# Performance work log

Hardware: AMD Instinct MI355X
Metric: run time of the kernel (lower is better)

## Reference

```python
import jax, jax.numpy as jnp
import numpy as np

N = 100000
E = 1600000
IN = 256
H = 4
D = 32           # n_hidden per head
C = 47           # n_classes per head in last layer
NEG_SLOPE = 0.2


def setup_inputs() -> dict:
    key = jax.random.key(0)
    ks = jax.random.split(key, 20)
    x = jax.random.normal(ks[0], (N, IN), dtype=jnp.float32)
    src = jax.random.randint(ks[1], (E,), 0, N, dtype=jnp.int32)
    dst = jax.random.randint(ks[2], (E,), 0, N, dtype=jnp.int32)
    s = 0.05
    inp = {"x": x, "src": src, "dst": dst}
    # layer 0: in 256 -> (H=4, D=32)
    inp["W0s"] = jax.random.normal(ks[3], (IN, H * D), dtype=jnp.float32) * s
    inp["W0d"] = jax.random.normal(ks[4], (IN, H * D), dtype=jnp.float32) * s
    inp["a0l"] = jax.random.normal(ks[5], (H, D), dtype=jnp.float32) * s
    inp["a0r"] = jax.random.normal(ks[6], (H, D), dtype=jnp.float32) * s
    inp["b0"] = jnp.zeros((H, D), dtype=jnp.float32)
    # layer 1: in 128 -> (4, 32)
    inp["W1s"] = jax.random.normal(ks[7], (H * D, H * D), dtype=jnp.float32) * s
    inp["W1d"] = jax.random.normal(ks[8], (H * D, H * D), dtype=jnp.float32) * s
    inp["a1l"] = jax.random.normal(ks[9], (H, D), dtype=jnp.float32) * s
    inp["a1r"] = jax.random.normal(ks[10], (H, D), dtype=jnp.float32) * s
    inp["b1"] = jnp.zeros((H, D), dtype=jnp.float32)
    # layer 2: in 128 -> (4, 47), no activation
    inp["W2s"] = jax.random.normal(ks[11], (H * D, H * C), dtype=jnp.float32) * s
    inp["W2d"] = jax.random.normal(ks[12], (H * D, H * C), dtype=jnp.float32) * s
    inp["a2l"] = jax.random.normal(ks[13], (H, C), dtype=jnp.float32) * s
    inp["a2r"] = jax.random.normal(ks[14], (H, C), dtype=jnp.float32) * s
    inp["b2"] = jnp.zeros((H, C), dtype=jnp.float32)
    return inp


def _gat_layer(h, src, dst, Ws, Wd, al, ar, b):
    # h: [N, F_in]; full-graph block so h_dst == h
    n = h.shape[0]
    heads, dout = al.shape
    fs = (h @ Ws).reshape(n, heads, dout)   # [N, H, D]
    fd = (h @ Wd).reshape(n, heads, dout)
    el = jnp.sum(fs * al, axis=-1)          # [N, H]
    er = jnp.sum(fd * ar, axis=-1)
    e = el[src] + er[dst]                   # [E, H]
    e = jnp.where(e > 0, e, NEG_SLOPE * e)  # leaky_relu
    # segment softmax over incoming edges of each dst node
    m = jax.lax.stop_gradient(jax.ops.segment_max(e, dst, num_segments=n))
    ez = jnp.exp(e - m[dst])
    denom = jax.ops.segment_sum(ez, dst, num_segments=n)
    alpha = ez / denom[dst]                 # [E, H]
    msg = fs[src] * alpha[:, :, None]       # [E, H, D]
    rst = jax.ops.segment_sum(msg, dst, num_segments=n)  # [N, H, D]
    return rst + b


def reference(x, src, dst,
              W0s, W0d, a0l, a0r, b0,
              W1s, W1d, a1l, a1r, b1,
              W2s, W2d, a2l, a2r, b2):
    h = _gat_layer(x, src, dst, W0s, W0d, a0l, a0r, b0)
    h = jax.nn.relu(h).reshape(h.shape[0], -1)           # flatten(1)
    h = _gat_layer(h, src, dst, W1s, W1d, a1l, a1r, b1)
    h = jax.nn.relu(h).reshape(h.shape[0], -1)
    h = _gat_layer(h, src, dst, W2s, W2d, a2l, a2r, b2)  # [N, H, C]
    h = h.mean(axis=1)                                   # mean over heads
    return jax.nn.log_softmax(h, axis=-1)
```

## Files before the change

### kernel.cpp

```cpp
#include <hip/hip_runtime.h>
#include <math.h>

#define NEG_SLOPE 0.2f

typedef _Float16 half2v __attribute__((ext_vector_type(2)));
typedef _Float16 half8 __attribute__((ext_vector_type(8)));
typedef float float4v __attribute__((ext_vector_type(4)));
typedef float float2v __attribute__((ext_vector_type(2)));

__device__ __forceinline__ float lrelu(float x) { return x > 0.f ? x : NEG_SLOPE * x; }

__device__ __forceinline__ float sel4(const float4 v, int h) {
  float r = v.x;
  r = (h == 1) ? v.y : r;
  r = (h == 2) ? v.z : r;
  r = (h == 3) ? v.w : r;
  return r;
}

__device__ __forceinline__ unsigned char f32_to_fp8(float a) {
  int v = __builtin_amdgcn_cvt_pk_fp8_f32(a, 0.f, 0, false);
  return (unsigned char)(v & 0xff);
}


__global__ void k_hist(const int* __restrict__ dst, int* __restrict__ cnt, int E) {
  int i = blockIdx.x * blockDim.x + threadIdx.x;
  if (i < E) atomicAdd(&cnt[dst[i]], 1);
}

__global__ __launch_bounds__(256) void k_offsets(const int* __restrict__ cnt,
                                                 int* __restrict__ row_start,
                                                 int* __restrict__ gcount, int N) {
  __shared__ int s[256];
  __shared__ int base;
  int tid = threadIdx.x;
  int i = blockIdx.x * 256 + tid;
  int c = (i < N) ? cnt[i] : 0;
  s[tid] = c;
  __syncthreads();
  for (int off = 1; off < 256; off <<= 1) {
    int v = 0;
    if (tid >= off) v = s[tid - off];
    __syncthreads();
    if (tid >= off) s[tid] += v;
    __syncthreads();
  }
  if (tid == 255) base = atomicAdd(gcount, s[255]);
  __syncthreads();
  if (i < N) row_start[i] = base + s[tid] - c;
}

__global__ void k_scatter(const int* __restrict__ src, const int* __restrict__ dst,
                          const int* __restrict__ row_start, int* __restrict__ fill,
                          int* __restrict__ srcs, int E) {
  int i = blockIdx.x * blockDim.x + threadIdx.x;
  if (i < E) {
    int d = dst[i];
    int p = row_start[d] + atomicAdd(&fill[d], 1);
    srcs[p] = src[i];
  }
}

__device__ __forceinline__ void wlr_one(const float* Ws, const float* Wd,
                                        const float* al, const float* ar,
                                        float* wlr, int K, int Dh, int i) {
  int M = 4 * Dh;
  int k = i >> 2, h = i & 3;
  float sl = 0.f, sr = 0.f;
  for (int d = 0; d < Dh; d++) {
    sl += Ws[(size_t)k * M + h * Dh + d] * al[h * Dh + d];
    sr += Wd[(size_t)k * M + h * Dh + d] * ar[h * Dh + d];
  }
  wlr[k * 8 + h] = sl;
  wlr[k * 8 + 4 + h] = sr;
}

__global__ __launch_bounds__(256) void k_prep(
    const float* __restrict__ W0s, const float* __restrict__ W0d,
    const float* __restrict__ a0l, const float* __restrict__ a0r,
    const float* __restrict__ W1s, const float* __restrict__ W1d,
    const float* __restrict__ a1l, const float* __restrict__ a1r,
    const float* __restrict__ W2s, const float* __restrict__ W2d,
    const float* __restrict__ a2l, const float* __restrict__ a2r,
    float* __restrict__ wlr0, float* __restrict__ wlr1, float* __restrict__ wlr2,
    _Float16* __restrict__ Wt0, _Float16* __restrict__ Wt1, _Float16* __restrict__ Wt2) {
  int i = blockIdx.x * 256 + threadIdx.x;
  if (i < 1024) {
    wlr_one(W0s, W0d, a0l, a0r, wlr0, 256, 32, i);
  } else if (i < 1536) {
    wlr_one(W1s, W1d, a1l, a1r, wlr1, 128, 32, i - 1024);
  } else if (i < 2048) {
    wlr_one(W2s, W2d, a2l, a2r, wlr2, 128, 47, i - 1536);
  } else if (i < 2048 + 32768) {
    int j = i - 2048;
    int m = j >> 8, k = j & 255;
    Wt0[j] = (_Float16)W0s[(size_t)k * 128 + m];
  } else if (i < 2048 + 32768 + 16384) {
    int j = i - (2048 + 32768);
    int m = j >> 7, k = j & 127;
    Wt1[j] = (_Float16)W1s[(size_t)k * 128 + m];
  } else if (i < 2048 + 32768 + 16384 + 24576) {
    int j = i - (2048 + 32768 + 16384);
    int r = j >> 7, k = j & 127;
    int h = r / 48, c = r % 48;
    float v = (c < 47) ? W2s[(size_t)k * 188 + 47 * h + c] : 0.f;
    Wt2[j] = (_Float16)v;
  }
}

template <int BN, typename AT>
__global__ __launch_bounds__(256) void k_gemm_mfma(const AT* __restrict__ A,
                                                   const _Float16* __restrict__ Bt,
                                                   const float* __restrict__ wlr,
                                                   unsigned char* __restrict__ C,
                                                   float* __restrict__ el,
                                                   float* __restrict__ er, int N, int K) {
  constexpr int NT = BN / 64;
  constexpr int ASZ = 4 * 64 * 8;
  constexpr int BSZ = (BN / 16) * 64 * 8;
  constexpr int SSZ = ASZ + BSZ;
  __shared__ __align__(16) _Float16 smem[SSZ];
  __shared__ float swlr[2048];
  _Float16* As = smem;
  _Float16* Bs = smem + ASZ;

  const int tid = threadIdx.x;
  const int lane = tid & 63;
  const int w = tid >> 6;
  const int row0 = blockIdx.x * 64;

  for (int i = tid; i < K * 8; i += 256) swlr[i] = wlr[i];
  __syncthreads();

  float4v acc[4][NT];
#pragma unroll
  for (int i = 0; i < 4; i++)
#pragma unroll
    for (int j = 0; j < NT; j++) acc[i][j] = (float4v){0.f, 0.f, 0.f, 0.f};
  float p[8] = {0, 0, 0, 0, 0, 0, 0, 0};

  const int ar_ = tid >> 2, aq = tid & 3;
  for (int k0 = 0; k0 < K; k0 += 32) {
    {
      int gr = row0 + ar_;
      float a8[8];
      if (gr < N) {
        if constexpr (sizeof(AT) == 4) {
          const float4* pp = (const float4*)&A[(size_t)gr * K + k0 + aq * 8];
          float4 u0 = pp[0], u1 = pp[1];
          a8[0] = u0.x; a8[1] = u0.y; a8[2] = u0.z; a8[3] = u0.w;
          a8[4] = u1.x; a8[5] = u1.y; a8[6] = u1.z; a8[7] = u1.w;
        } else {
          half8 hv = *(const half8*)&A[(size_t)gr * K + k0 + aq * 8];
#pragma unroll
          for (int j = 0; j < 8; j++) a8[j] = (float)hv[j];
        }
      } else {
#pragma unroll
        for (int j = 0; j < 8; j++) a8[j] = 0.f;
      }
      half8 v;
#pragma unroll
      for (int j = 0; j < 8; j++) v[j] = (_Float16)a8[j];
      *(half8*)&As[(size_t)(((ar_ >> 4) * 64) + (ar_ & 15) + 16 * aq) * 8] = v;
#pragma unroll
      for (int j = 0; j < 8; j++) {
        const float av = a8[j];
        const float* wp = &swlr[(k0 + aq * 8 + j) * 8];
        float4 w0 = *(const float4*)wp;
        float4 w1 = *(const float4*)(wp + 4);
        p[0] += av * w0.x; p[1] += av * w0.y; p[2] += av * w0.z; p[3] += av * w0.w;
        p[4] += av * w1.x; p[5] += av * w1.y; p[6] += av * w1.z; p[7] += av * w1.w;
      }
    }
#pragma unroll
    for (int i = 0; i < NT; i++) {
      int idx = tid + i * 256;
      int n = idx >> 2, q = idx & 3;
      half8 v = *(const half8*)&Bt[(size_t)n * K + k0 + q * 8];
      *(half8*)&Bs[(size_t)((n >> 4) * 64 + (n & 15) + 16 * q) * 8] = v;
    }
    __syncthreads();
    half8 af[4];
#pragma unroll
    for (int mt = 0; mt < 4; mt++) af[mt] = *(half8*)&As[(size_t)(mt * 64 + lane) * 8];
#pragma unroll
    for (int nt = 0; nt < NT; nt++) {
      half8 bf = *(half8*)&Bs[(size_t)((w * NT + nt) * 64 + lane) * 8];
#pragma unroll
      for (int mt = 0; mt < 4; mt++)
        acc[mt][nt] = __builtin_amdgcn_mfma_f32_16x16x32_f16(af[mt], bf, acc[mt][nt], 0, 0, 0);
    }
    __syncthreads();
  }

#pragma unroll
  for (int j = 0; j < 8; j++) swlr[(ar_ * 4 + aq) * 8 + j] = p[j];

  unsigned char* cs = (unsigned char*)smem;
  const int quad = lane >> 4;
#pragma unroll
  for (int mt = 0; mt < 4; mt++)
#pragma unroll
    for (int nt = 0; nt < NT; nt++)
#pragma unroll
      for (int reg = 0; reg < 4; reg++) {
        int r = mt * 16 + quad * 4 + reg;
        int cc = (w * NT + nt) * 16 + (lane & 15);
        cs[r * BN + cc] = f32_to_fp8(acc[mt][nt][reg]);
      }
  __syncthreads();
  if (tid < 64) {
    int gr = row0 + tid;
    if (gr < N) {
      float e[8];
#pragma unroll
      for (int j = 0; j < 8; j++)
        e[j] = swlr[(tid * 4 + 0) * 8 + j] + swlr[(tid * 4 + 1) * 8 + j] +
               swlr[(tid * 4 + 2) * 8 + j] + swlr[(tid * 4 + 3) * 8 + j];
      *(float4*)&el[(size_t)gr * 4] = make_float4(e[0], e[1], e[2], e[3]);
      *(float4*)&er[(size_t)gr * 4] = make_float4(e[4], e[5], e[6], e[7]);
    }
  }
  constexpr int PER = (64 * BN) / (256 * 16);
  const uint4* s4 = (const uint4*)cs;
#pragma unroll
  for (int i = 0; i < PER; i++) {
    int idx = tid + i * 256;
    int r = idx / (BN / 16), c16 = idx % (BN / 16);
    int gr = row0 + r;
    if (gr < N) *(uint4*)&C[(size_t)gr * BN + c16 * 16] = s4[idx];
  }
}

__global__ __launch_bounds__(256) void k_edge_mid(
    const unsigned char* __restrict__ F, const float* __restrict__ el,
    const float* __restrict__ er, const int* __restrict__ row_start,
    const int* __restrict__ cnt, const int* __restrict__ srcs,
    const float* __restrict__ bias, _Float16* __restrict__ hout, int N) {
  __shared__ float sEz[4][64][4];
  __shared__ int sU[4][64];
  int lane = threadIdx.x & 63;
  int w = threadIdx.x >> 6;
  int v = blockIdx.x * 4 + w;
  if (v >= N) return;
  int start = row_start[v], deg = cnt[v];
  float4 erv = *(const float4*)&er[(size_t)v * 4];
  const int g = lane >> 4;
  const int fl = lane & 15;
  const int h = fl >> 2;
  float acc[8] = {0, 0, 0, 0, 0, 0, 0, 0};
  float4 lsum = make_float4(0.f, 0.f, 0.f, 0.f);

  for (int c = 0; c < deg; c += 64) {
    int take = min(64, deg - c);
    if (lane < take) {
      int u = srcs[start + c + lane];
      float4 e = *(const float4*)&el[(size_t)u * 4];
      float4 ez;
      ez.x = __expf(lrelu(e.x + erv.x));
      ez.y = __expf(lrelu(e.y + erv.y));
      ez.z = __expf(lrelu(e.z + erv.z));
      ez.w = __expf(lrelu(e.w + erv.w));
      lsum.x += ez.x; lsum.y += ez.y; lsum.z += ez.z; lsum.w += ez.w;
      sU[w][lane] = u;
      *(float4*)&sEz[w][lane][0] = ez;
    }
    for (int kk = g; kk < take; kk += 4) {
      int u = sU[w][kk];
      float ezh = sEz[w][kk][h];
      uint2 d = *(const uint2*)&F[(size_t)u * 128 + 8 * fl];
      float2v c0 = __builtin_amdgcn_cvt_pk_f32_fp8((int)d.x, false);
      float2v c1 = __builtin_amdgcn_cvt_pk_f32_fp8((int)d.x, true);
      float2v c2 = __builtin_amdgcn_cvt_pk_f32_fp8((int)d.y, false);
      float2v c3 = __builtin_amdgcn_cvt_pk_f32_fp8((int)d.y, true);
      acc[0] += ezh * c0.x; acc[1] += ezh * c0.y;
      acc[2] += ezh * c1.x; acc[3] += ezh * c1.y;
      acc[4] += ezh * c2.x; acc[5] += ezh * c2.y;
      acc[6] += ezh * c3.x; acc[7] += ezh * c3.y;
    }
  }
#pragma unroll
  for (int j = 0; j < 8; j++) {
    acc[j] += __shfl_xor(acc[j], 16);
    acc[j] += __shfl_xor(acc[j], 32);
  }
#pragma unroll
  for (int msk = 1; msk < 64; msk <<= 1) {
    lsum.x += __shfl_xor(lsum.x, msk);
    lsum.y += __shfl_xor(lsum.y, msk);
    lsum.z += __shfl_xor(lsum.z, msk);
    lsum.w += __shfl_xor(lsum.w, msk);
  }
  if (g == 0) {
    float inv = (deg > 0) ? 1.f / sel4(lsum, h) : 0.f;
    const float4* bp = (const float4*)&bias[8 * fl];
    float4 b0v = bp[0], b1v = bp[1];
    float bb[8] = {b0v.x, b0v.y, b0v.z, b0v.w, b1v.x, b1v.y, b1v.z, b1v.w};
    half8 o;
#pragma unroll
    for (int j = 0; j < 8; j++) o[j] = (_Float16)fmaxf(fmaf(acc[j], inv, bb[j]), 0.f);
    *(half8*)&hout[(size_t)v * 128 + 8 * fl] = o;
  }
}

__global__ __launch_bounds__(256) void k_edge_final(
    const unsigned char* __restrict__ F, const float* __restrict__ el,
    const float* __restrict__ er, const int* __restrict__ row_start,
    const int* __restrict__ cnt, const int* __restrict__ srcs,
    const float* __restrict__ b2, float* __restrict__ out, int N) {
  __shared__ float sEz[4][64][4];
  __shared__ int sU[4][64];
  __shared__ float red[4][192];
  int lane = threadIdx.x & 63;
  int w = threadIdx.x >> 6;
  int v = blockIdx.x * 4 + w;
  if (v >= N) return;
  int start = row_start[v], deg = cnt[v];
  float4 erv = *(const float4*)&er[(size_t)v * 4];
  const int sub = lane >> 5;
  const int l24 = lane & 31;
  const bool act = l24 < 24;
  const int h = l24 / 6;
  const int j6 = l24 % 6;
  const int foff = 48 * h + 8 * j6;
  float acc[8] = {0, 0, 0, 0, 0, 0, 0, 0};
  float4 lsum = make_float4(0.f, 0.f, 0.f, 0.f);

  for (int c = 0; c < deg; c += 64) {
    int take = min(64, deg - c);
    if (lane < take) {
      int u = srcs[start + c + lane];
      float4 e = *(const float4*)&el[(size_t)u * 4];
      float4 ez;
      ez.x = __expf(lrelu(e.x + erv.x));
      ez.y = __expf(lrelu(e.y + erv.y));
      ez.z = __expf(lrelu(e.z + erv.z));
      ez.w = __expf(lrelu(e.w + erv.w));
      lsum.x += ez.x; lsum.y += ez.y; lsum.z += ez.z; lsum.w += ez.w;
      sU[w][lane] = u;
      *(float4*)&sEz[w][lane][0] = ez;
    }
    if (act) {
      for (int kk = sub; kk < take; kk += 2) {
        int u = sU[w][kk];
        float ezh = sEz[w][kk][h];
        uint2 d = *(const uint2*)&F[(size_t)u * 192 + foff];
        float2v c0 = __builtin_amdgcn_cvt_pk_f32_fp8((int)d.x, false);
        float2v c1 = __builtin_amdgcn_cvt_pk_f32_fp8((int)d.x, true);
        float2v c2 = __builtin_amdgcn_cvt_pk_f32_fp8((int)d.y, false);
        float2v c3 = __builtin_amdgcn_cvt_pk_f32_fp8((int)d.y, true);
        acc[0] += ezh * c0.x; acc[1] += ezh * c0.y;
        acc[2] += ezh * c1.x; acc[3] += ezh * c1.y;
        acc[4] += ezh * c2.x; acc[5] += ezh * c2.y;
        acc[6] += ezh * c3.x; acc[7] += ezh * c3.y;
      }
    }
  }
#pragma unroll
  for (int j = 0; j < 8; j++) acc[j] += __shfl_xor(acc[j], 32);
#pragma unroll
  for (int msk = 1; msk < 64; msk <<= 1) {
    lsum.x += __shfl_xor(lsum.x, msk);
    lsum.y += __shfl_xor(lsum.y, msk);
    lsum.z += __shfl_xor(lsum.z, msk);
    lsum.w += __shfl_xor(lsum.w, msk);
  }
  if (act && sub == 0) {
    float inv = (deg > 0) ? 1.f / sel4(lsum, h) : 0.f;
#pragma unroll
    for (int j = 0; j < 8; j++) {
      int cc = 8 * j6 + j;
      float bv = (cc < 47) ? b2[47 * h + cc] : 0.f;
      red[w][foff + j] = fmaf(acc[j], inv, bv);
    }
  }
  __syncthreads();
  float g = -INFINITY;
  if (lane < 47)
    g = 0.25f * (red[w][lane] + red[w][lane + 48] + red[w][lane + 96] + red[w][lane + 144]);
  float gm = g;
#pragma unroll
  for (int msk = 1; msk < 64; msk <<= 1) gm = fmaxf(gm, __shfl_xor(gm, msk));
  float ex = (lane < 47) ? __expf(g - gm) : 0.f;
  float s = ex;
#pragma unroll
  for (int msk = 1; msk < 64; msk <<= 1) s += __shfl_xor(s, msk);
  if (lane < 47) out[(size_t)v * 47 + lane] = g - gm - __logf(s);
}

extern "C" void kernel_launch(void* const* d_in, const int* in_sizes, int n_in,
                              void* d_out, int out_size, void* d_ws, size_t ws_size,
                              hipStream_t stream) {
  const float* x = (const float*)d_in[0];
  const int* src = (const int*)d_in[1];
  const int* dst = (const int*)d_in[2];
  const float* W0s = (const float*)d_in[3];
  const float* W0d = (const float*)d_in[4];
  const float* a0l = (const float*)d_in[5];
  const float* a0r = (const float*)d_in[6];
  const float* b0 = (const float*)d_in[7];
  const float* W1s = (const float*)d_in[8];
  const float* W1d = (const float*)d_in[9];
  const float* a1l = (const float*)d_in[10];
  const float* a1r = (const float*)d_in[11];
  const float* b1 = (const float*)d_in[12];
  const float* W2s = (const float*)d_in[13];
  const float* W2d = (const float*)d_in[14];
  const float* a2l = (const float*)d_in[15];
  const float* a2r = (const float*)d_in[16];
  const float* b2 = (const float*)d_in[17];
  float* out = (float*)d_out;

  const int N = in_sizes[0] / 256;
  const int E = in_sizes[1];

  char* w = (char*)d_ws;
  size_t off = 0;
  auto alloc = [&](size_t bytes) -> void* {
    void* p = w + off;
    off += (bytes + 255) & ~(size_t)255;
    return p;
  };
  int* gcount = (int*)alloc(4);
  int* cnt = (int*)alloc((size_t)N * 4);
  int* fill = (int*)alloc((size_t)N * 4);
  size_t zbytes = off;
  int* row_start = (int*)alloc((size_t)N * 4);
  int* srcs = (int*)alloc((size_t)E * 4);
  float* wlr0 = (float*)alloc(256 * 8 * 4);
  float* wlr1 = (float*)alloc(128 * 8 * 4);
  float* wlr2 = (float*)alloc(128 * 8 * 4);
  _Float16* Wt0 = (_Float16*)alloc(128 * 256 * 2);
  _Float16* Wt1 = (_Float16*)alloc(128 * 128 * 2);
  _Float16* Wt2 = (_Float16*)alloc(192 * 128 * 2);
  float* el = (float*)alloc((size_t)N * 4 * 4);
  float* er = (float*)alloc((size_t)N * 4 * 4);
  unsigned char* F = (unsigned char*)alloc((size_t)N * 192);
  _Float16* Ha = (_Float16*)alloc((size_t)N * 128 * 2);
  _Float16* Hc = (_Float16*)alloc((size_t)N * 128 * 2);
  (void)ws_size;

  hipMemsetAsync(d_ws, 0, zbytes, stream);
  k_hist<<<(E + 255) / 256, 256, 0, stream>>>(dst, cnt, E);
  k_offsets<<<(N + 255) / 256, 256, 0, stream>>>(cnt, row_start, gcount, N);
  k_scatter<<<(E + 255) / 256, 256, 0, stream>>>(src, dst, row_start, fill, srcs, E);
  k_prep<<<(75776 + 255) / 256, 256, 0, stream>>>(W0s, W0d, a0l, a0r, W1s, W1d, a1l, a1r,
                                                  W2s, W2d, a2l, a2r, wlr0, wlr1, wlr2,
                                                  Wt0, Wt1, Wt2);

  int gemm_grid = (N + 63) / 64;
  int node_grid = (N + 3) / 4;

  k_gemm_mfma<128, float><<<gemm_grid, 256, 0, stream>>>(x, Wt0, wlr0, F, el, er, N, 256);
  k_edge_mid<<<node_grid, 256, 0, stream>>>(F, el, er, row_start, cnt, srcs, b0, Ha, N);

  k_gemm_mfma<128, _Float16><<<gemm_grid, 256, 0, stream>>>(Ha, Wt1, wlr1, F, el, er, N, 128);
  k_edge_mid<<<node_grid, 256, 0, stream>>>(F, el, er, row_start, cnt, srcs, b1, Hc, N);

  k_gemm_mfma<192, _Float16><<<gemm_grid, 256, 0, stream>>>(Hc, Wt2, wlr2, F, el, er, N, 128);
  k_edge_final<<<node_grid, 256, 0, stream>>>(F, el, er, row_start, cnt, srcs, b2, out, N);
}
```

Before: 683.0 us.

## Widen edge gathers to 16-byte loads with software prefetch and packed FMA

The mid and final edge-aggregation kernels now gather 16 fp8 features per lane with uint4 loads instead of 8 with uint2. More edges are handled in parallel per wavefront (8 in the mid kernel, 5 in the final one), and the next edge's row is loaded before the current one is accumulated, using float2 packed multiply-adds. The cross-lane reductions are rebuilt for the new lane mapping, the bias is folded in after the head mean, and the block-wide __syncthreads is dropped. This trades more shuffle reduction steps and idle lanes in the final kernel for fewer, wider memory transactions and more loads in flight. Dropping the barrier across a wave's shared-memory writes and reads relies on wavefront-level ordering.

```diff
diff --git a/kernel.cpp b/kernel.cpp
--- a/kernel.cpp
+++ b/kernel.cpp
@@ -21,6 +21,19 @@
 __device__ __forceinline__ unsigned char f32_to_fp8(float a) {
   int v = __builtin_amdgcn_cvt_pk_fp8_f32(a, 0.f, 0, false);
   return (unsigned char)(v & 0xff);
+}
+
+__device__ __forceinline__ void acc16(float2v acc[8], uint4 d, float ez) {
+  float2v ez2 = {ez, ez};
+  float2v c;
+  c = __builtin_amdgcn_cvt_pk_f32_fp8((int)d.x, false); acc[0] += ez2 * c;
+  c = __builtin_amdgcn_cvt_pk_f32_fp8((int)d.x, true);  acc[1] += ez2 * c;
+  c = __builtin_amdgcn_cvt_pk_f32_fp8((int)d.y, false); acc[2] += ez2 * c;
+  c = __builtin_amdgcn_cvt_pk_f32_fp8((int)d.y, true);  acc[3] += ez2 * c;
+  c = __builtin_amdgcn_cvt_pk_f32_fp8((int)d.z, false); acc[4] += ez2 * c;
+  c = __builtin_amdgcn_cvt_pk_f32_fp8((int)d.z, true);  acc[5] += ez2 * c;
+  c = __builtin_amdgcn_cvt_pk_f32_fp8((int)d.w, false); acc[6] += ez2 * c;
+  c = __builtin_amdgcn_cvt_pk_f32_fp8((int)d.w, true);  acc[7] += ez2 * c;
 }
 
 
@@ -247,10 +260,12 @@
   if (v >= N) return;
   int start = row_start[v], deg = cnt[v];
   float4 erv = *(const float4*)&er[(size_t)v * 4];
-  const int g = lane >> 4;
-  const int fl = lane & 15;
-  const int h = fl >> 2;
-  float acc[8] = {0, 0, 0, 0, 0, 0, 0, 0};
+  const int g8 = lane >> 3;
+  const int sl = lane & 7;
+  const int h = sl >> 1;
+  float2v acc2[8];
+#pragma unroll
+  for (int i = 0; i < 8; i++) acc2[i] = (float2v){0.f, 0.f};
   float4 lsum = make_float4(0.f, 0.f, 0.f, 0.f);
 
   for (int c = 0; c < deg; c += 64) {
@@ -267,25 +282,28 @@
       sU[w][lane] = u;
       *(float4*)&sEz[w][lane][0] = ez;
     }
-    for (int kk = g; kk < take; kk += 4) {
-      int u = sU[w][kk];
-      float ezh = sEz[w][kk][h];
-      uint2 d = *(const uint2*)&F[(size_t)u * 128 + 8 * fl];
-      float2v c0 = __builtin_amdgcn_cvt_pk_f32_fp8((int)d.x, false);
-      float2v c1 = __builtin_amdgcn_cvt_pk_f32_fp8((int)d.x, true);
-      float2v c2 = __builtin_amdgcn_cvt_pk_f32_fp8((int)d.y, false);
-      float2v c3 = __builtin_amdgcn_cvt_pk_f32_fp8((int)d.y, true);
-      acc[0] += ezh * c0.x; acc[1] += ezh * c0.y;
-      acc[2] += ezh * c1.x; acc[3] += ezh * c1.y;
-      acc[4] += ezh * c2.x; acc[5] += ezh * c2.y;
-      acc[6] += ezh * c3.x; acc[7] += ezh * c3.y;
-    }
-  }
-#pragma unroll
-  for (int j = 0; j < 8; j++) {
-    acc[j] += __shfl_xor(acc[j], 16);
-    acc[j] += __shfl_xor(acc[j], 32);
-  }
+    int kk = g8;
+    if (kk < take) {
+      int u0 = sU[w][kk];
+      float ez0 = sEz[w][kk][h];
+      uint4 d0 = *(const uint4*)&F[((unsigned)u0 << 7) + 16u * (unsigned)sl];
+      for (kk += 8; kk < take; kk += 8) {
+        int u1 = sU[w][kk];
+        float ez1 = sEz[w][kk][h];
+        uint4 d1 = *(const uint4*)&F[((unsigned)u1 << 7) + 16u * (unsigned)sl];
+        acc16(acc2, d0, ez0);
+        d0 = d1; ez0 = ez1;
+      }
+      acc16(acc2, d0, ez0);
+    }
+  }
+#pragma unroll
+  for (int m = 8; m < 64; m <<= 1)
+#pragma unroll
+    for (int i = 0; i < 8; i++) {
+      acc2[i].x += __shfl_xor(acc2[i].x, m);
+      acc2[i].y += __shfl_xor(acc2[i].y, m);
+    }
 #pragma unroll
   for (int msk = 1; msk < 64; msk <<= 1) {
     lsum.x += __shfl_xor(lsum.x, msk);
@@ -293,15 +311,25 @@
     lsum.z += __shfl_xor(lsum.z, msk);
     lsum.w += __shfl_xor(lsum.w, msk);
   }
-  if (g == 0) {
+  if (g8 == 0) {
     float inv = (deg > 0) ? 1.f / sel4(lsum, h) : 0.f;
-    const float4* bp = (const float4*)&bias[8 * fl];
-    float4 b0v = bp[0], b1v = bp[1];
-    float bb[8] = {b0v.x, b0v.y, b0v.z, b0v.w, b1v.x, b1v.y, b1v.z, b1v.w};
-    half8 o;
-#pragma unroll
-    for (int j = 0; j < 8; j++) o[j] = (_Float16)fmaxf(fmaf(acc[j], inv, bb[j]), 0.f);
-    *(half8*)&hout[(size_t)v * 128 + 8 * fl] = o;
+    const float4* bp = (const float4*)&bias[16 * sl];
+    float4 b0v = bp[0], b1v = bp[1], b2v = bp[2], b3v = bp[3];
+    float bb[16] = {b0v.x, b0v.y, b0v.z, b0v.w, b1v.x, b1v.y, b1v.z, b1v.w,
+                    b2v.x, b2v.y, b2v.z, b2v.w, b3v.x, b3v.y, b3v.z, b3v.w};
+    half8 o0, o1;
+#pragma unroll
+    for (int j = 0; j < 8; j++) {
+      float a = acc2[j >> 1][j & 1];
+      o0[j] = (_Float16)fmaxf(fmaf(a, inv, bb[j]), 0.f);
+    }
+#pragma unroll
+    for (int j = 0; j < 8; j++) {
+      float a = acc2[(j + 8) >> 1][j & 1];
+      o1[j] = (_Float16)fmaxf(fmaf(a, inv, bb[j + 8]), 0.f);
+    }
+    *(half8*)&hout[(size_t)v * 128 + 16 * sl] = o0;
+    *(half8*)&hout[(size_t)v * 128 + 16 * sl + 8] = o1;
   }
 }
 
@@ -319,13 +347,13 @@
   if (v >= N) return;
   int start = row_start[v], deg = cnt[v];
   float4 erv = *(const float4*)&er[(size_t)v * 4];
-  const int sub = lane >> 5;
-  const int l24 = lane & 31;
-  const bool act = l24 < 24;
-  const int h = l24 / 6;
-  const int j6 = l24 % 6;
-  const int foff = 48 * h + 8 * j6;
-  float acc[8] = {0, 0, 0, 0, 0, 0, 0, 0};
+  const int e0 = lane / 12;
+  const int sl = lane - e0 * 12;
+  const bool act = e0 < 5;
+  const int h = sl / 3;
+  float2v acc2[8];
+#pragma unroll
+  for (int i = 0; i < 8; i++) acc2[i] = (float2v){0.f, 0.f};
   float4 lsum = make_float4(0.f, 0.f, 0.f, 0.f);
 
   for (int c = 0; c < deg; c += 64) {
@@ -343,23 +371,32 @@
       *(float4*)&sEz[w][lane][0] = ez;
     }
     if (act) {
-      for (int kk = sub; kk < take; kk += 2) {
-        int u = sU[w][kk];
-        float ezh = sEz[w][kk][h];
-        uint2 d = *(const uint2*)&F[(size_t)u * 192 + foff];
-        float2v c0 = __builtin_amdgcn_cvt_pk_f32_fp8((int)d.x, false);
-        float2v c1 = __builtin_amdgcn_cvt_pk_f32_fp8((int)d.x, true);
-        float2v c2 = __builtin_amdgcn_cvt_pk_f32_fp8((int)d.y, false);
-        float2v c3 = __builtin_amdgcn_cvt_pk_f32_fp8((int)d.y, true);
-        acc[0] += ezh * c0.x; acc[1] += ezh * c0.y;
-        acc[2] += ezh * c1.x; acc[3] += ezh * c1.y;
-        acc[4] += ezh * c2.x; acc[5] += ezh * c2.y;
-        acc[6] += ezh * c3.x; acc[7] += ezh * c3.y;
+      int kk = e0;
+      if (kk < take) {
+        int u0 = sU[w][kk];
+        float ez0 = sEz[w][kk][h];
+        uint4 d0 = *(const uint4*)&F[(unsigned)u0 * 192u + 16u * (unsigned)sl];
+        for (kk += 5; kk < take; kk += 5) {
+          int u1 = sU[w][kk];
+          float ez1 = sEz[w][kk][h];
+          uint4 d1 = *(const uint4*)&F[(unsigned)u1 * 192u + 16u * (unsigned)sl];
+          acc16(acc2, d0, ez0);
+          d0 = d1; ez0 = ez1;
+        }
+        acc16(acc2, d0, ez0);
       }
     }
   }
 #pragma unroll
-  for (int j = 0; j < 8; j++) acc[j] += __shfl_xor(acc[j], 32);
+  for (int i = 0; i < 8; i++) {
+    float ax = acc2[i].x, ay = acc2[i].y;
+    float t1x = ax + __shfl(ax, lane + 12);
+    float t1y = ay + __shfl(ay, lane + 12);
+    float t2x = t1x + __shfl(t1x, lane + 24);
+    float t2y = t1y + __shfl(t1y, lane + 24);
+    acc2[i].x = t2x + __shfl(ax, lane + 48);
+    acc2[i].y = t2y + __shfl(ay, lane + 48);
+  }
 #pragma unroll
   for (int msk = 1; msk < 64; msk <<= 1) {
     lsum.x += __shfl_xor(lsum.x, msk);
@@ -367,19 +404,20 @@
     lsum.z += __shfl_xor(lsum.z, msk);
     lsum.w += __shfl_xor(lsum.w, msk);
   }
-  if (act && sub == 0) {
+  if (lane < 12) {
     float inv = (deg > 0) ? 1.f / sel4(lsum, h) : 0.f;
 #pragma unroll
     for (int j = 0; j < 8; j++) {
-      int cc = 8 * j6 + j;
-      float bv = (cc < 47) ? b2[47 * h + cc] : 0.f;
-      red[w][foff + j] = fmaf(acc[j], inv, bv);
-    }
-  }
-  __syncthreads();
+      red[w][sl * 16 + 2 * j] = acc2[j].x * inv;
+      red[w][sl * 16 + 2 * j + 1] = acc2[j].y * inv;
+    }
+  }
   float g = -INFINITY;
-  if (lane < 47)
-    g = 0.25f * (red[w][lane] + red[w][lane + 48] + red[w][lane + 96] + red[w][lane + 144]);
+  if (lane < 47) {
+    float s4 = red[w][lane] + red[w][lane + 48] + red[w][lane + 96] + red[w][lane + 144];
+    float bsum = b2[lane] + b2[47 + lane] + b2[94 + lane] + b2[141 + lane];
+    g = 0.25f * (s4 + bsum);
+  }
   float gm = g;
 #pragma unroll
   for (int msk = 1; msk < 64; msk <<= 1) gm = fmaxf(gm, __shfl_xor(gm, msk));
```

Result: slower. 712.8 us (+4.4%).

## Split layer-0 edge aggregation into two head-half passes with cached edge scores

Applied to the files above, without the earlier changes.

Layer 0's edge kernel is split into two passes. Each pass gathers only half of every source node's FP8 feature row (64 of 128 bytes), so the gathered working set per pass is smaller and more likely to stay in cache. The first pass computes the exp scores and stores them with the source index in a packed per-edge buffer that reuses the Hc scratch space, and it writes per-node inverse denominators. The second pass reads the packed buffer for the other two heads instead of recomputing. The cost is an extra launch and extra per-edge writes and reads of the 16-byte packed records.

```diff
diff --git a/kernel.cpp b/kernel.cpp
--- a/kernel.cpp
+++ b/kernel.cpp
@@ -305,6 +305,155 @@
   }
 }
 
+__global__ __launch_bounds__(256) void k_edge_midA(
+    const unsigned char* __restrict__ F, const float* __restrict__ el,
+    const float* __restrict__ er, const int* __restrict__ row_start,
+    const int* __restrict__ cnt, const int* __restrict__ srcs,
+    const float* __restrict__ bias, _Float16* __restrict__ hout,
+    uint4* __restrict__ ezPk, float* __restrict__ invd, int N) {
+  __shared__ float sEz[4][64][2];
+  __shared__ int sU[4][64];
+  int lane = threadIdx.x & 63;
+  int w = threadIdx.x >> 6;
+  int v = blockIdx.x * 4 + w;
+  if (v >= N) return;
+  int start = row_start[v], deg = cnt[v];
+  float4 erv = *(const float4*)&er[(size_t)v * 4];
+  const int g = lane >> 3;
+  const int fl = lane & 7;
+  const int h = fl >> 2;
+  float acc[8] = {0, 0, 0, 0, 0, 0, 0, 0};
+  float4 lsum = make_float4(0.f, 0.f, 0.f, 0.f);
+
+  for (int c = 0; c < deg; c += 64) {
+    int take = min(64, deg - c);
+    if (lane < take) {
+      int u = srcs[start + c + lane];
+      float4 e = *(const float4*)&el[(size_t)u * 4];
+      float4 ez;
+      ez.x = __expf(lrelu(e.x + erv.x));
+      ez.y = __expf(lrelu(e.y + erv.y));
+      ez.z = __expf(lrelu(e.z + erv.z));
+      ez.w = __expf(lrelu(e.w + erv.w));
+      lsum.x += ez.x; lsum.y += ez.y; lsum.z += ez.z; lsum.w += ez.w;
+      sU[w][lane] = u;
+      sEz[w][lane][0] = ez.x;
+      sEz[w][lane][1] = ez.y;
+      half2v e01 = {(_Float16)ez.x, (_Float16)ez.y};
+      half2v e23 = {(_Float16)ez.z, (_Float16)ez.w};
+      uint4 pk;
+      pk.x = (unsigned)u;
+      pk.y = __builtin_bit_cast(unsigned, e01);
+      pk.z = __builtin_bit_cast(unsigned, e23);
+      pk.w = 0u;
+      ezPk[(size_t)(start + c + lane)] = pk;
+    }
+    for (int kk = g; kk < take; kk += 8) {
+      int u = sU[w][kk];
+      float ezh = sEz[w][kk][h];
+      uint2 d = *(const uint2*)&F[((size_t)u << 7) + 8u * (unsigned)fl];
+      float2v c0 = __builtin_amdgcn_cvt_pk_f32_fp8((int)d.x, false);
+      float2v c1 = __builtin_amdgcn_cvt_pk_f32_fp8((int)d.x, true);
+      float2v c2 = __builtin_amdgcn_cvt_pk_f32_fp8((int)d.y, false);
+      float2v c3 = __builtin_amdgcn_cvt_pk_f32_fp8((int)d.y, true);
+      acc[0] += ezh * c0.x; acc[1] += ezh * c0.y;
+      acc[2] += ezh * c1.x; acc[3] += ezh * c1.y;
+      acc[4] += ezh * c2.x; acc[5] += ezh * c2.y;
+      acc[6] += ezh * c3.x; acc[7] += ezh * c3.y;
+    }
+  }
+#pragma unroll
+  for (int j = 0; j < 8; j++) {
+    acc[j] += __shfl_xor(acc[j], 8);
+    acc[j] += __shfl_xor(acc[j], 16);
+    acc[j] += __shfl_xor(acc[j], 32);
+  }
+#pragma unroll
+  for (int msk = 1; msk < 64; msk <<= 1) {
+    lsum.x += __shfl_xor(lsum.x, msk);
+    lsum.y += __shfl_xor(lsum.y, msk);
+    lsum.z += __shfl_xor(lsum.z, msk);
+    lsum.w += __shfl_xor(lsum.w, msk);
+  }
+  if (lane == 0) {
+    float4 iv;
+    iv.x = (deg > 0) ? 1.f / lsum.x : 0.f;
+    iv.y = (deg > 0) ? 1.f / lsum.y : 0.f;
+    iv.z = (deg > 0) ? 1.f / lsum.z : 0.f;
+    iv.w = (deg > 0) ? 1.f / lsum.w : 0.f;
+    *(float4*)&invd[(size_t)v * 4] = iv;
+  }
+  if (g == 0) {
+    float inv = (deg > 0) ? 1.f / ((h == 0) ? lsum.x : lsum.y) : 0.f;
+    const float4* bp = (const float4*)&bias[8 * fl];
+    float4 b0v = bp[0], b1v = bp[1];
+    float bb[8] = {b0v.x, b0v.y, b0v.z, b0v.w, b1v.x, b1v.y, b1v.z, b1v.w};
+    half8 o;
+#pragma unroll
+    for (int j = 0; j < 8; j++) o[j] = (_Float16)fmaxf(fmaf(acc[j], inv, bb[j]), 0.f);
+    *(half8*)&hout[(size_t)v * 128 + 8 * fl] = o;
+  }
+}
+
+__global__ __launch_bounds__(256) void k_edge_midB(
+    const unsigned char* __restrict__ F, const int* __restrict__ row_start,
+    const int* __restrict__ cnt, const uint4* __restrict__ ezPk,
+    const float* __restrict__ invd, const float* __restrict__ bias,
+    _Float16* __restrict__ hout, int N) {
+  __shared__ float sEz[4][64][2];
+  __shared__ int sU[4][64];
+  int lane = threadIdx.x & 63;
+  int w = threadIdx.x >> 6;
+  int v = blockIdx.x * 4 + w;
+  if (v >= N) return;
+  int start = row_start[v], deg = cnt[v];
+  float4 iv = *(const float4*)&invd[(size_t)v * 4];
+  const int g = lane >> 3;
+  const int fl = lane & 7;
+  const int h2 = fl >> 2;
+  float acc[8] = {0, 0, 0, 0, 0, 0, 0, 0};
+
+  for (int c = 0; c < deg; c += 64) {
+    int take = min(64, deg - c);
+    if (lane < take) {
+      uint4 pk = ezPk[(size_t)(start + c + lane)];
+      half2v e23 = __builtin_bit_cast(half2v, pk.z);
+      sU[w][lane] = (int)pk.x;
+      sEz[w][lane][0] = (float)e23[0];
+      sEz[w][lane][1] = (float)e23[1];
+    }
+    for (int kk = g; kk < take; kk += 8) {
+      int u = sU[w][kk];
+      float ezh = sEz[w][kk][h2];
+      uint2 d = *(const uint2*)&F[((size_t)u << 7) + 64u + 8u * (unsigned)fl];
+      float2v c0 = __builtin_amdgcn_cvt_pk_f32_fp8((int)d.x, false);
+      float2v c1 = __builtin_amdgcn_cvt_pk_f32_fp8((int)d.x, true);
+      float2v c2 = __builtin_amdgcn_cvt_pk_f32_fp8((int)d.y, false);
+      float2v c3 = __builtin_amdgcn_cvt_pk_f32_fp8((int)d.y, true);
+      acc[0] += ezh * c0.x; acc[1] += ezh * c0.y;
+      acc[2] += ezh * c1.x; acc[3] += ezh * c1.y;
+      acc[4] += ezh * c2.x; acc[5] += ezh * c2.y;
+      acc[6] += ezh * c3.x; acc[7] += ezh * c3.y;
+    }
+  }
+#pragma unroll
+  for (int j = 0; j < 8; j++) {
+    acc[j] += __shfl_xor(acc[j], 8);
+    acc[j] += __shfl_xor(acc[j], 16);
+    acc[j] += __shfl_xor(acc[j], 32);
+  }
+  if (g == 0) {
+    float inv = (h2 == 0) ? iv.z : iv.w;
+    const float4* bp = (const float4*)&bias[64 + 8 * fl];
+    float4 b0v = bp[0], b1v = bp[1];
+    float bb[8] = {b0v.x, b0v.y, b0v.z, b0v.w, b1v.x, b1v.y, b1v.z, b1v.w};
+    half8 o;
+#pragma unroll
+    for (int j = 0; j < 8; j++) o[j] = (_Float16)fmaxf(fmaf(acc[j], inv, bb[j]), 0.f);
+    *(half8*)&hout[(size_t)v * 128 + 64 + 8 * fl] = o;
+  }
+}
+
 __global__ __launch_bounds__(256) void k_edge_final(
     const unsigned char* __restrict__ F, const float* __restrict__ el,
     const float* __restrict__ er, const int* __restrict__ row_start,
@@ -437,9 +586,11 @@
   _Float16* Wt2 = (_Float16*)alloc(192 * 128 * 2);
   float* el = (float*)alloc((size_t)N * 4 * 4);
   float* er = (float*)alloc((size_t)N * 4 * 4);
+  float* invd = (float*)alloc((size_t)N * 4 * 4);
   unsigned char* F = (unsigned char*)alloc((size_t)N * 192);
   _Float16* Ha = (_Float16*)alloc((size_t)N * 128 * 2);
   _Float16* Hc = (_Float16*)alloc((size_t)N * 128 * 2);
+  uint4* ezPk = (uint4*)Hc;
   (void)ws_size;
 
   hipMemsetAsync(d_ws, 0, zbytes, stream);
@@ -454,7 +605,9 @@
   int node_grid = (N + 3) / 4;
 
   k_gemm_mfma<128, float><<<gemm_grid, 256, 0, stream>>>(x, Wt0, wlr0, F, el, er, N, 256);
-  k_edge_mid<<<node_grid, 256, 0, stream>>>(F, el, er, row_start, cnt, srcs, b0, Ha, N);
+  k_edge_midA<<<node_grid, 256, 0, stream>>>(F, el, er, row_start, cnt, srcs, b0, Ha,
+                                             ezPk, invd, N);
+  k_edge_midB<<<node_grid, 256, 0, stream>>>(F, row_start, cnt, ezPk, invd, b0, Ha, N);
 
   k_gemm_mfma<128, _Float16><<<gemm_grid, 256, 0, stream>>>(Ha, Wt1, wlr1, F, el, er, N, 128);
   k_edge_mid<<<node_grid, 256, 0, stream>>>(F, el, er, row_start, cnt, srcs, b1, Hc, N);
```

After: 725.0 us. 6.1% more time.
